# Optimization experiments

Measured on AMD Instinct MI355X. Metric: run time of the kernel, lower is better.

The kernel has to match this reference:

```python
import jax, jax.numpy as jnp
import numpy as np

NUM_HEADS = 4
WINDOW = 3

def setup_inputs() -> dict:
    key = jax.random.key(0)
    ks = jax.random.split(key, 6)
    B, V, C, H, W = 4, 6, 256, 32, 32
    s = 0.02
    return {
        "x": jax.random.normal(ks[0], (B, V, C, H, W), jnp.float32),
        "Wq": jax.random.normal(ks[1], (C, C), jnp.float32) * s,
        "bq": jnp.zeros((C,), jnp.float32),
        "Wk": jax.random.normal(ks[2], (V * C, C), jnp.float32) * s,
        "bk": jnp.zeros((C,), jnp.float32),
        "Wv": jax.random.normal(ks[3], (V * C, C), jnp.float32) * s,
        "bv": jnp.zeros((C,), jnp.float32),
        "Wo": jax.random.normal(ks[4], (C, C), jnp.float32) * s,
        "bo": jnp.zeros((C,), jnp.float32),
    }

def reference(x, Wq, bq, Wk, bk, Wv, bv, Wo, bo):
    B, V, C, H, W = x.shape
    HW = H * W
    S = HW * V  # query sequence length
    nh = NUM_HEADS
    hd = C // nh
    # q: [B, V, H, W, C] -> [B, S, C]
    q_in = jnp.transpose(x, (0, 1, 3, 4, 2)).reshape(B, S, C)
    # k/v input: [B, H, W, V, C] -> [B, HW, V*C]
    kv_in = jnp.transpose(x, (0, 3, 4, 1, 2)).reshape(B, HW, V * C)
    q = q_in @ Wq + bq
    k = kv_in @ Wk + bk
    v = kv_in @ Wv + bv
    q = q.reshape(B, S, nh, hd).transpose(0, 2, 1, 3)    # [B, nh, S, hd]
    k = k.reshape(B, HW, nh, hd).transpose(0, 2, 1, 3)   # [B, nh, HW, hd]
    v = v.reshape(B, HW, nh, hd).transpose(0, 2, 1, 3)   # [B, nh, HW, hd]
    logits = jnp.einsum("bhqd,bhkd->bhqk", q, k) / jnp.sqrt(jnp.float32(hd))
    # Faithful mask: row i has ones in columns [max(0,i-W), i+W] (clipped to HW cols);
    # it is ADDED as mask * -1e9, masking OUT the diagonal window (as in source).
    i = jnp.arange(S)[:, None]
    j = jnp.arange(HW)[None, :]
    mask = ((j >= i - WINDOW) & (j < i + WINDOW + 1)).astype(logits.dtype)
    logits = logits + mask * (-1e9)
    attn = jax.nn.softmax(logits, axis=-1)
    out = jnp.einsum("bhqk,bhkd->bhqd", attn, v)         # [B, nh, S, hd]
    out = out.transpose(0, 2, 1, 3).reshape(B, S, C)
    out = out @ Wo + bo
    return x.reshape(B * V, C, H, W) + out.reshape(B * V, C, H, W)
```

## Files before the change

kernel.cpp:

```cpp
#include <hip/hip_runtime.h>
#include <cstddef>

namespace {

constexpr int B=4, V=6, C=256, HWS=1024, S=6144, NH=4, HD=64, VC=1536;

typedef short short8  __attribute__((ext_vector_type(8)));
typedef short short4v __attribute__((ext_vector_type(4)));
typedef float f32x4   __attribute__((ext_vector_type(4)));

__device__ inline short f2bf(float f){
  union{float f; unsigned u;} v; v.f=f;
  unsigned r = v.u + 0x7fffu + ((v.u>>16)&1u);
  return (short)(r>>16);
}
__device__ inline unsigned fbits(float f){
  union{float f; unsigned u;} v; v.f=f; return v.u;
}

typedef const __attribute__((address_space(1))) unsigned* gas_t;
typedef __attribute__((address_space(3))) unsigned* las_t;
__device__ inline void gll(const void* g, void* l){
  __builtin_amdgcn_global_load_lds((gas_t)g, (las_t)l, 16, 0, 0);
}

__device__ inline void tr_tile(const float* in, int inRow, short* out, int outRow,
                               int r0, int c0, int t){
  const int tx=t&15, ty=t>>4;
  float a[4][4];
  #pragma unroll
  for(int i=0;i<4;i++){
    const float4 f=*(const float4*)(in + (size_t)(r0+ty*4+i)*inRow + c0 + tx*4);
    a[i][0]=f.x; a[i][1]=f.y; a[i][2]=f.z; a[i][3]=f.w;
  }
  #pragma unroll
  for(int j=0;j<4;j++){
    short4v o4;
    #pragma unroll
    for(int i=0;i<4;i++) o4[i]=f2bf(a[i][j]);
    *(short4v*)(out + (size_t)(c0+tx*4+j)*outRow + r0+ty*4) = o4;
  }
}

__global__ __launch_bounds__(256) void prep(const float* __restrict__ x,
                                            const float* __restrict__ Wq, const float* __restrict__ Wk,
                                            const float* __restrict__ Wv, const float* __restrict__ Wo,
                                            short* __restrict__ xb, short* __restrict__ WqT,
                                            short* __restrict__ WkT, short* __restrict__ WvT,
                                            short* __restrict__ WoT){
  const int blk=blockIdx.x;
  if(blk<1536){
    const int bx=blk&15, by=(blk>>4)&3, bv=blk>>6;
    tr_tile(x + (size_t)bv*C*HWS, HWS, xb + (size_t)bv*HWS*C, C, by*64, bx*64, threadIdx.x);
  } else {
    const int idx=blk-1536;
    const int tile=idx%96, z=idx/96;
    const float* in; short* out; int R;
    if(z==0){in=Wq; out=WqT; R=C;}
    else if(z==1){in=Wo; out=WoT; R=C;}
    else if(z==2){in=Wk; out=WkT; R=VC;}
    else         {in=Wv; out=WvT; R=VC;}
    const int tilesC=C/64, ntiles=(R/64)*tilesC;
    if(tile>=ntiles) return;
    tr_tile(in, C, out, R, (tile/tilesC)*64, (tile%tilesC)*64, threadIdx.x);
  }
}

template<int MODE>
__device__ inline void qo_body(const short* __restrict__ A, const short* __restrict__ BT,
                               const float* __restrict__ bias, const float* __restrict__ xres,
                               void* __restrict__ outv, short* sh, int n0, int r0){
  const int t=threadIdx.x, lane=t&63, w=t>>6, quad=lane>>4, ln=lane&15;
  f32x4 acc[2][4];
  #pragma unroll
  for(int rt=0;rt<2;rt++)
    #pragma unroll
    for(int nt=0;nt<4;nt++) acc[rt][nt]=(f32x4)0.f;

  const int sr=w*8+(lane>>3), scc=(lane&7)*8;
  auto stage=[&](int it,int bufi){
    const int k0=it*64;
    short* dst = sh + bufi*12288;
    const short* Asrc = A + (size_t)r0*C + k0;
    #pragma unroll
    for(int cc=0; cc<4; cc++)
      gll(Asrc + (size_t)(sr+cc*32)*C + scc, dst + cc*2048 + w*512);
    const short* Bsrc = BT + (size_t)n0*C + k0;
    gll(Bsrc + (size_t)sr*C + scc,      dst + 8192 + w*512);
    gll(Bsrc + (size_t)(sr+32)*C + scc, dst + 8192 + 2048 + w*512);
  };

  stage(0,0);
  __syncthreads();
  for(int it=0; it<4; it++){
    if(it<3) stage(it+1,(it+1)&1);
    const short* As_=sh+(it&1)*12288;
    const short* Bs_=As_+8192;
    #pragma unroll
    for(int s=0;s<2;s++){
      const short8 af0=*(const short8*)&As_[(w*32+ln)*64    + s*32+quad*8];
      const short8 af1=*(const short8*)&As_[(w*32+16+ln)*64 + s*32+quad*8];
      #pragma unroll
      for(int nt=0;nt<4;nt++){
        const short8 bf=*(const short8*)&Bs_[(nt*16+ln)*64 + s*32+quad*8];
        acc[0][nt]=__builtin_amdgcn_mfma_f32_16x16x32_bf16(af0,bf,acc[0][nt],0,0,0);
        acc[1][nt]=__builtin_amdgcn_mfma_f32_16x16x32_bf16(af1,bf,acc[1][nt],0,0,0);
      }
    }
    __syncthreads();
  }

  constexpr float QSCALE = 0.18033688011112042f;
  float bcol[4];
  #pragma unroll
  for(int nt=0;nt<4;nt++) bcol[nt]=bias[n0+nt*16+ln];
  #pragma unroll
  for(int rt=0;rt<2;rt++)
    #pragma unroll
    for(int nt=0;nt<4;nt++)
      #pragma unroll
      for(int i=0;i<4;i++){
        const int row=r0+w*32+rt*16+quad*4+i, col=n0+nt*16+ln;
        const float vv=acc[rt][nt][i]+bcol[nt];
        if constexpr(MODE==0) ((short*)outv)[(size_t)row*C+col]=f2bf(vv*QSCALE);
        else ((float*)outv)[(size_t)row*C+col]=vv + xres[(size_t)row*C+col];
      }
}

__global__ __launch_bounds__(256) void proj(const short* __restrict__ xb,
                                            const short* __restrict__ WqT, const short* __restrict__ WkT,
                                            const short* __restrict__ WvT,
                                            const float* __restrict__ bq, const float* __restrict__ bk,
                                            const float* __restrict__ bv,
                                            short* __restrict__ qb, short* __restrict__ Kpack,
                                            short* __restrict__ Vpack){
  __shared__ __align__(16) short sh[24576];
  const int blk=blockIdx.x;
  const int t=threadIdx.x, lane=t&63, w=t>>6, quad=lane>>4, ln=lane&15;

  if(blk>=256){
    const int qblk=blk-256;
    qo_body<0>(xb, WqT, bq, nullptr, qb, sh, (qblk&3)*64, (qblk>>2)*128);
    return;
  }

  const int n0=(blk&3)*64, r0=(blk>>2)*64;
  const int b=r0>>10, hw0=r0&1023;
  const int h=n0>>6, bh=b*NH+h;

  f32x4 ak[4], av[4];
  #pragma unroll
  for(int nt=0;nt<4;nt++){ ak[nt]=(f32x4)0.f; av[nt]=(f32x4)0.f; }

  const int sr=w*8+(lane>>3), scc=(lane&7)*8;
  auto stageKV=[&](int it,int bufi){
    const int k0=it*64, v=k0>>8, c0=k0&255;
    short* dst = sh + bufi*12288;
    const short* As_src = xb + (size_t)((b*V+v)*HWS + hw0)*C + c0;
    gll(As_src + (size_t)sr*C + scc,       dst + w*512);
    gll(As_src + (size_t)(sr+32)*C + scc,  dst + 2048 + w*512);
    const short* Bk_src = WkT + (size_t)n0*VC + k0;
    gll(Bk_src + (size_t)sr*VC + scc,      dst + 4096 + w*512);
    gll(Bk_src + (size_t)(sr+32)*VC + scc, dst + 4096 + 2048 + w*512);
    const short* Bv_src = WvT + (size_t)n0*VC + k0;
    gll(Bv_src + (size_t)sr*VC + scc,      dst + 8192 + w*512);
    gll(Bv_src + (size_t)(sr+32)*VC + scc, dst + 8192 + 2048 + w*512);
  };

  stageKV(0,0);
  __syncthreads();
  for(int it=0; it<24; it++){
    if(it<23) stageKV(it+1,(it+1)&1);
    const short* As_=sh+(it&1)*12288;
    const short* Bk_=As_+4096;
    const short* Bv_=As_+8192;
    #pragma unroll
    for(int s=0;s<2;s++){
      const short8 af=*(const short8*)&As_[(w*16+ln)*64 + s*32+quad*8];
      #pragma unroll
      for(int nt=0;nt<4;nt++){
        const short8 kf=*(const short8*)&Bk_[(nt*16+ln)*64 + s*32+quad*8];
        const short8 vf=*(const short8*)&Bv_[(nt*16+ln)*64 + s*32+quad*8];
        ak[nt]=__builtin_amdgcn_mfma_f32_16x16x32_bf16(af,kf,ak[nt],0,0,0);
        av[nt]=__builtin_amdgcn_mfma_f32_16x16x32_bf16(af,vf,av[nt],0,0,0);
      }
    }
    __syncthreads();
  }

  float bkc[4], bvc[4];
  #pragma unroll
  for(int nt=0;nt<4;nt++){ bkc[nt]=bk[n0+nt*16+ln]; bvc[nt]=bv[n0+nt*16+ln]; }

  {
    short* vq = Vpack + ((size_t)(bh*64 + (hw0>>4) + w))*1024;
    #pragma unroll
    for(int nt=0;nt<4;nt++){
      short4v vp;
      #pragma unroll
      for(int i=0;i<4;i++) vp[i]=f2bf(av[nt][i]+bvc[nt]);
      *(short4v*)(vq + nt*256 + lane*4) = vp;
    }
  }

  __syncthreads();
  #pragma unroll
  for(int nt=0;nt<4;nt++)
    #pragma unroll
    for(int i=0;i<4;i++)
      sh[(w*16+quad*4+i)*72 + nt*16+ln] = f2bf(ak[nt][i]+bkc[nt]);
  __syncthreads();
  {
    short* kp = Kpack + ((size_t)(bh*64 + (hw0>>4) + w))*1024;
    #pragma unroll
    for(int half=0; half<2; half++){
      const short8 f = *(short8*)&sh[(w*16+ln)*72 + half*32 + quad*8];
      *(short8*)(kp + half*512 + lane*8) = f;
    }
  }
}

__global__ __launch_bounds__(512,4) void attn_k(const short* __restrict__ q, const short* __restrict__ Kpack,
                                                const short* __restrict__ Vpack, short* __restrict__ ao){
  __shared__ __align__(16) char smem[34816];
  short* KV   = (short*)smem;
  float* obuf = (float*)smem;
  float* lbuf = (float*)(smem + 33792);

  const int blk=blockIdx.x;
  const int bh=(blk&7)*2 + ((blk>>3)&1);
  const int qt=blk>>4;
  const int b=bh>>2, h=bh&3;
  const int s0=qt*128;
  const int t=threadIdx.x, lane=t&63, w=t>>6, quad=lane>>4, ln=lane&15;
  const int wq=w&3, wk=w>>2;

  short8 qf[2][2];
  #pragma unroll
  for(int ntl=0;ntl<2;ntl++)
    #pragma unroll
    for(int s=0;s<2;s++)
      qf[ntl][s]=*(const short8*)&q[(size_t)(b*S+s0+wq*32+ntl*16+ln)*C + h*HD + s*32+quad*8];

  f32x4 o[4][2];
  #pragma unroll
  for(int dt=0;dt<4;dt++)
    #pragma unroll
    for(int ntl=0;ntl<2;ntl++) o[dt][ntl]=(f32x4)0.f;
  f32x4 l4[2];
  l4[0]=(f32x4)0.f; l4[1]=(f32x4)0.f;

  const short* Kt = Kpack + (size_t)bh*65536;
  const short* Vt = Vpack + (size_t)bh*65536;
  const f32x4 z4=(f32x4)0.f;
  const int rb = s0 + wq*32;

  gll(Kt + w*512 + lane*8, KV + w*512);
  gll(Vt + w*512 + lane*8, KV + 4096 + w*512);
  __syncthreads();

  #pragma unroll 1
  for(int TI=0; TI<16; TI++){
    if(TI<15){
      const int nb=(TI+1)&1;
      gll(Kt + (size_t)(TI+1)*4096 + w*512 + lane*8, KV + nb*8192 + w*512);
      gll(Vt + (size_t)(TI+1)*4096 + w*512 + lane*8, KV + nb*8192 + 4096 + w*512);
    }
    const short* Kb = KV + (TI&1)*8192;
    const short* Vb = Kb + 4096;

    const short8 kf00=*(const short8*)&Kb[wk*2048 + lane*8];
    const short8 kf01=*(const short8*)&Kb[wk*2048 + 512 + lane*8];
    const short8 kf10=*(const short8*)&Kb[wk*2048 + 1024 + lane*8];
    const short8 kf11=*(const short8*)&Kb[wk*2048 + 1536 + lane*8];

    f32x4 sa[2][2];
    #pragma unroll
    for(int ntl=0;ntl<2;ntl++){
      sa[0][ntl]=__builtin_amdgcn_mfma_f32_16x16x32_bf16(kf00,qf[ntl][0],z4,0,0,0);
      sa[0][ntl]=__builtin_amdgcn_mfma_f32_16x16x32_bf16(kf01,qf[ntl][1],sa[0][ntl],0,0,0);
      sa[1][ntl]=__builtin_amdgcn_mfma_f32_16x16x32_bf16(kf10,qf[ntl][0],z4,0,0,0);
      sa[1][ntl]=__builtin_amdgcn_mfma_f32_16x16x32_bf16(kf11,qf[ntl][1],sa[1][ntl],0,0,0);
    }

    short4v vf[2][4];
    #pragma unroll
    for(int kt=0;kt<2;kt++)
      #pragma unroll
      for(int dt=0;dt<4;dt++)
        vf[kt][dt]=*(const short4v*)&Vb[wk*2048 + kt*1024 + dt*256 + lane*4];

    const int kmin=TI*64 + wk*32;
    if(kmin+31 >= rb-3 && kmin <= rb+34){
      #pragma unroll
      for(int kt=0;kt<2;kt++)
        #pragma unroll
        for(int ntl=0;ntl<2;ntl++){
          const int ig=rb+ntl*16+ln;
          #pragma unroll
          for(int i=0;i<4;i++){
            const int jg=kmin+kt*16+quad*4+i;
            if((unsigned)(jg-ig+3)<=6u) sa[kt][ntl][i]=-100.f;
          }
        }
    }

    short4v pt[2][2];
    #pragma unroll
    for(int kt=0;kt<2;kt++)
      #pragma unroll
      for(int ntl=0;ntl<2;ntl++){
        f32x4 pv;
        #pragma unroll
        for(int i=0;i<4;i++) pv[i]=__builtin_amdgcn_exp2f(sa[kt][ntl][i]);
        l4[ntl]+=pv;
        union{ short4v s; unsigned u[2]; } P;
        P.u[0]=__builtin_amdgcn_perm(fbits(pv[1]), fbits(pv[0]), 0x07060302u);
        P.u[1]=__builtin_amdgcn_perm(fbits(pv[3]), fbits(pv[2]), 0x07060302u);
        pt[kt][ntl]=P.s;
      }

    #pragma unroll
    for(int kt=0;kt<2;kt++)
      #pragma unroll
      for(int dt=0;dt<4;dt++)
        #pragma unroll
        for(int ntl=0;ntl<2;ntl++)
          o[dt][ntl]=__builtin_amdgcn_mfma_f32_16x16x16bf16_1k(vf[kt][dt],pt[kt][ntl],o[dt][ntl],0,0,0);

    __syncthreads();
  }

  float l[2];
  #pragma unroll
  for(int ntl=0;ntl<2;ntl++){
    l[ntl]=l4[ntl][0]+l4[ntl][1]+l4[ntl][2]+l4[ntl][3];
    l[ntl]+=__shfl_xor(l[ntl],16);
    l[ntl]+=__shfl_xor(l[ntl],32);
  }
  if(quad==0){
    lbuf[w*32+ln]    = l[0];
    lbuf[w*32+16+ln] = l[1];
  }
  if(wk==0){
    #pragma unroll
    for(int dt=0;dt<4;dt++)
      #pragma unroll
      for(int ntl=0;ntl<2;ntl++)
        #pragma unroll
        for(int i=0;i<4;i++)
          obuf[(dt*16+quad*4+i)*132 + wq*32+ntl*16+ln] = o[dt][ntl][i];
  }
  __syncthreads();
  if(wk==1){
    #pragma unroll
    for(int dt=0;dt<4;dt++)
      #pragma unroll
      for(int ntl=0;ntl<2;ntl++)
        #pragma unroll
        for(int i=0;i<4;i++)
          obuf[(dt*16+quad*4+i)*132 + wq*32+ntl*16+ln] += o[dt][ntl][i];
  }
  __syncthreads();

  {
    const int row=t>>2, dg=t&3;
    const float linv=1.0f/(lbuf[(row>>5)*32 + (row&31)] + lbuf[(4+(row>>5))*32 + (row&31)]);
    short tmp[16];
    #pragma unroll
    for(int j=0;j<16;j++) tmp[j]=f2bf(obuf[(dg*16+j)*132+row]*linv);
    short* op = ao + (size_t)(b*S+s0+row)*C + h*HD + dg*16;
    *(short8*)op     = *(short8*)&tmp[0];
    *(short8*)(op+8) = *(short8*)&tmp[8];
  }
}

__global__ __launch_bounds__(256) void o_gemm(const short* __restrict__ A, const short* __restrict__ BT,
                                              const float* __restrict__ bias, const float* __restrict__ xres,
                                              float* __restrict__ out){
  __shared__ __align__(16) short sh[24576];
  qo_body<1>(A, BT, bias, xres, out, sh, (int)(blockIdx.x&3)*64, (int)(blockIdx.x>>2)*128);
}

}

extern "C" void kernel_launch(void* const* d_in, const int* in_sizes, int n_in,
                              void* d_out, int out_size, void* d_ws, size_t ws_size,
                              hipStream_t stream) {
  const float* x  = (const float*)d_in[0];
  const float* Wq = (const float*)d_in[1];
  const float* bq = (const float*)d_in[2];
  const float* Wk = (const float*)d_in[3];
  const float* bk = (const float*)d_in[4];
  const float* Wv = (const float*)d_in[5];
  const float* bv = (const float*)d_in[6];
  const float* Wo = (const float*)d_in[7];
  const float* bo = (const float*)d_in[8];
  float* out = (float*)d_out;

  char* p = (char*)d_ws;
  const size_t szBS=(size_t)B*S*C*2, szK=(size_t)B*HWS*C*2;
  short* xb   =(short*)p; p+=szBS;
  short* qb   =(short*)p; p+=szBS;
  short* aob  =(short*)p; p+=szBS;
  short* Kpack=(short*)p; p+=szK;
  short* Vpack=(short*)p; p+=szK;
  short* WqT=(short*)p; p+=(size_t)C*C*2;
  short* WoT=(short*)p; p+=(size_t)C*C*2;
  short* WkT=(short*)p; p+=(size_t)C*VC*2;
  short* WvT=(short*)p; p+=(size_t)C*VC*2;

  prep<<<dim3(1920), 256, 0, stream>>>(x, Wq,Wk,Wv,Wo, xb, WqT,WkT,WvT,WoT);
  proj<<<dim3(1024), 256, 0, stream>>>(xb, WqT,WkT,WvT, bq,bk,bv, qb, Kpack, Vpack);
  attn_k<<<dim3(B*NH*(S/128)), 512, 0, stream>>>(qb, Kpack, Vpack, aob);
  o_gemm<<<dim3(4*((B*S)/128)), 256, 0, stream>>>(aob, WoT, bo, x, out);
}
```

Baseline: 168.0 us.

## Load K/V fragments directly from global memory instead of LDS double-buffering

The attention kernel no longer stages K and V tiles through shared memory with async global-to-LDS copies and per-iteration barriers. Each wave now reads its K and V fragments straight from global memory (relying on L2/cache reuse across the four query-wave groups), which removes the __syncthreads in the loop. It also wraps the MFMA blocks in s_setprio raises to favour matrix issue across waves. The cost is more global and cache traffic, since K/V tiles are re-read by every wave rather than once per block, and load latency is no longer hidden by explicit prefetch.

```diff
diff --git a/kernel.cpp b/kernel.cpp
--- a/kernel.cpp
+++ b/kernel.cpp
@@ -223,7 +223,6 @@
 __global__ __launch_bounds__(512,4) void attn_k(const short* __restrict__ q, const short* __restrict__ Kpack,
                                                 const short* __restrict__ Vpack, short* __restrict__ ao){
   __shared__ __align__(16) char smem[34816];
-  short* KV   = (short*)smem;
   float* obuf = (float*)smem;
   float* lbuf = (float*)(smem + 33792);
 
@@ -250,31 +249,29 @@
   f32x4 l4[2];
   l4[0]=(f32x4)0.f; l4[1]=(f32x4)0.f;
 
-  const short* Kt = Kpack + (size_t)bh*65536;
-  const short* Vt = Vpack + (size_t)bh*65536;
+  const short* Kb0 = Kpack + (size_t)bh*65536 + wk*2048;
+  const short* Vb0 = Vpack + (size_t)bh*65536 + wk*2048;
   const f32x4 z4=(f32x4)0.f;
   const int rb = s0 + wq*32;
 
-  gll(Kt + w*512 + lane*8, KV + w*512);
-  gll(Vt + w*512 + lane*8, KV + 4096 + w*512);
-  __syncthreads();
-
   #pragma unroll 1
   for(int TI=0; TI<16; TI++){
-    if(TI<15){
-      const int nb=(TI+1)&1;
-      gll(Kt + (size_t)(TI+1)*4096 + w*512 + lane*8, KV + nb*8192 + w*512);
-      gll(Vt + (size_t)(TI+1)*4096 + w*512 + lane*8, KV + nb*8192 + 4096 + w*512);
-    }
-    const short* Kb = KV + (TI&1)*8192;
-    const short* Vb = Kb + 4096;
-
-    const short8 kf00=*(const short8*)&Kb[wk*2048 + lane*8];
-    const short8 kf01=*(const short8*)&Kb[wk*2048 + 512 + lane*8];
-    const short8 kf10=*(const short8*)&Kb[wk*2048 + 1024 + lane*8];
-    const short8 kf11=*(const short8*)&Kb[wk*2048 + 1536 + lane*8];
+    const short* Kb = Kb0 + TI*4096;
+    const short* Vb = Vb0 + TI*4096;
+
+    const short8 kf00=*(const short8*)&Kb[lane*8];
+    const short8 kf01=*(const short8*)&Kb[512 + lane*8];
+    const short8 kf10=*(const short8*)&Kb[1024 + lane*8];
+    const short8 kf11=*(const short8*)&Kb[1536 + lane*8];
+    short4v vf[2][4];
+    #pragma unroll
+    for(int kt=0;kt<2;kt++)
+      #pragma unroll
+      for(int dt=0;dt<4;dt++)
+        vf[kt][dt]=*(const short4v*)&Vb[kt*1024 + dt*256 + lane*4];
 
     f32x4 sa[2][2];
+    __builtin_amdgcn_s_setprio(1);
     #pragma unroll
     for(int ntl=0;ntl<2;ntl++){
       sa[0][ntl]=__builtin_amdgcn_mfma_f32_16x16x32_bf16(kf00,qf[ntl][0],z4,0,0,0);
@@ -282,13 +279,7 @@
       sa[1][ntl]=__builtin_amdgcn_mfma_f32_16x16x32_bf16(kf10,qf[ntl][0],z4,0,0,0);
       sa[1][ntl]=__builtin_amdgcn_mfma_f32_16x16x32_bf16(kf11,qf[ntl][1],sa[1][ntl],0,0,0);
     }
-
-    short4v vf[2][4];
-    #pragma unroll
-    for(int kt=0;kt<2;kt++)
-      #pragma unroll
-      for(int dt=0;dt<4;dt++)
-        vf[kt][dt]=*(const short4v*)&Vb[wk*2048 + kt*1024 + dt*256 + lane*4];
+    __builtin_amdgcn_s_setprio(0);
 
     const int kmin=TI*64 + wk*32;
     if(kmin+31 >= rb-3 && kmin <= rb+34){
@@ -320,6 +311,7 @@
         pt[kt][ntl]=P.s;
       }
 
+    __builtin_amdgcn_s_setprio(1);
     #pragma unroll
     for(int kt=0;kt<2;kt++)
       #pragma unroll
@@ -327,8 +319,7 @@
         #pragma unroll
         for(int ntl=0;ntl<2;ntl++)
           o[dt][ntl]=__builtin_amdgcn_mfma_f32_16x16x16bf16_1k(vf[kt][dt],pt[kt][ntl],o[dt][ntl],0,0,0);
-
-    __syncthreads();
+    __builtin_amdgcn_s_setprio(0);
   }
 
   float l[2];
```

Result: slower. 175.2 us (+4.3%).
